# Kernel optimization log

Measured on AMD Instinct MI355X. Metric: run time of the kernel, lower is better.

## Reference

```python
import jax, jax.numpy as jnp
import numpy as np

USER_N = 100000
ITEM_N = 20000
CONCEPT_N = 128
NB_MOD_MAX = 12
M = NB_MOD_MAX + 2  # nb_mod_max_plus_sent
B = 131072


def setup_inputs() -> dict:
    key = jax.random.key(0)
    ks = jax.random.split(key, 6)
    user_ids = jax.random.randint(ks[0], (B,), 0, USER_N)
    item_ids = jax.random.randint(ks[1], (B,), 0, ITEM_N)
    concept_ids = jax.random.randint(ks[2], (B,), 0, CONCEPT_N)
    users_emb_weight = jax.random.normal(ks[3], (USER_N, CONCEPT_N), jnp.float32)
    item_resp_emb_weight = jax.random.normal(ks[4], (ITEM_N * M, CONCEPT_N), jnp.float32)
    # per-item number of modalities in [2, nb_mod_max]
    nb_modalities = jax.random.randint(ks[5], (ITEM_N,), 2, NB_MOD_MAX + 1)
    # mask[item, c] = 0 for c in [1, nb_modalities[item]], +inf elsewhere (matches __init__)
    cols = jnp.arange(M)
    mask = jnp.where((cols[None, :] >= 1) & (cols[None, :] <= nb_modalities[:, None]),
                     0.0, jnp.inf).astype(jnp.float32)
    return dict(user_ids=user_ids, item_ids=item_ids, concept_ids=concept_ids,
                users_emb_weight=users_emb_weight,
                item_resp_emb_weight=item_resp_emb_weight,
                mask=mask, nb_modalities=nb_modalities)


def reference(user_ids, item_ids, concept_ids, users_emb_weight,
              item_resp_emb_weight, mask, nb_modalities):
    m = mask.shape[1]  # nb_mod_max + 2
    # im_idx buffer: item*M + arange(M), then gathered by item_ids
    im_idx = item_ids[:, None] * m + jnp.arange(m)        # [B, M]
    im_emb = item_resp_emb_weight[im_idx]                 # [B, M, C]
    u_emb = users_emb_weight[user_ids]                    # [B, C]
    diff = u_emb[:, None, :] - im_emb                     # [B, M, C]
    p_uim = jnp.sum(diff * diff, axis=2)                  # [B, M]
    idx = jnp.argmin(p_uim + mask[item_ids], axis=1)      # [B]
    nb = nb_modalities[item_ids]                          # [B]
    # mod_to_resp: ((idx - 1) / (nb - 1)) + 1
    return (idx - 1).astype(jnp.float32) / (nb - 1).astype(jnp.float32) + 1.0
```

## Files before the change

kernel.cpp:

```cpp
#include <hip/hip_runtime.h>
#include <math.h>


#define M_TOT 14
#define CDIM 128
#define TAU 0.05f
#define XSTR 68

__global__ void impact_hist(const int* __restrict__ item_ids,
                            int* __restrict__ hist, int B) {
    int i = blockIdx.x * blockDim.x + threadIdx.x;
    int i4 = i * 4;
    if (i4 + 3 < B) {
        int4 v = *(const int4*)(item_ids + i4);
        atomicAdd(&hist[v.x], 1);
        atomicAdd(&hist[v.y], 1);
        atomicAdd(&hist[v.z], 1);
        atomicAdd(&hist[v.w], 1);
    } else {
        for (int k = i4; k < B; ++k) atomicAdd(&hist[item_ids[k]], 1);
    }
}

__global__ __launch_bounds__(256) void impact_scan_part(
    const int* __restrict__ hist, int* __restrict__ cursor,
    int* __restrict__ bsum, int n) {
    __shared__ int sd[256];
    int t = threadIdx.x;
    int k = blockIdx.x * 256 + t;
    int v = (k < n) ? hist[k] : 0;
    sd[t] = v;
    __syncthreads();
#pragma unroll
    for (int off = 1; off < 256; off <<= 1) {
        int x = (t >= off) ? sd[t - off] : 0;
        __syncthreads();
        sd[t] += x;
        __syncthreads();
    }
    if (k < n) cursor[k] = sd[t] - v;
    if (t == 255) bsum[blockIdx.x] = sd[255];
}

__global__ __launch_bounds__(256) void impact_scatter(
    const int* __restrict__ item_ids,
    const int* __restrict__ user_ids,
    const int* __restrict__ nb_mod,
    int* __restrict__ cursor,
    const int* __restrict__ bsum, int nblk,
    int4* __restrict__ s4, int B)
{
    __shared__ int bo[128];
    int t = threadIdx.x;
    int v0 = 0;
    if (t < 128) {
        v0 = (t < nblk) ? bsum[t] : 0;
        bo[t] = v0;
    }
    __syncthreads();
#pragma unroll
    for (int off = 1; off < 128; off <<= 1) {
        int x = (t < 128 && t >= off) ? bo[t - off] : 0;
        __syncthreads();
        if (t < 128) bo[t] += x;
        __syncthreads();
    }
    int ex = (t < 128) ? bo[t] - v0 : 0;
    __syncthreads();
    if (t < 128) bo[t] = ex;
    __syncthreads();

    int i = blockIdx.x * blockDim.x + t;
    int i4 = i * 4;
    if (i4 + 3 < B) {
        int4 it = *(const int4*)(item_ids + i4);
        int4 us = *(const int4*)(user_ids + i4);
        int n0 = nb_mod[it.x], n1 = nb_mod[it.y];
        int n2 = nb_mod[it.z], n3 = nb_mod[it.w];
        int p0 = atomicAdd(&cursor[it.x], 1) + bo[it.x >> 8];
        int p1 = atomicAdd(&cursor[it.y], 1) + bo[it.y >> 8];
        int p2 = atomicAdd(&cursor[it.z], 1) + bo[it.z >> 8];
        int p3 = atomicAdd(&cursor[it.w], 1) + bo[it.w >> 8];
        s4[p0] = make_int4(i4,     us.x, it.x, n0);
        s4[p1] = make_int4(i4 + 1, us.y, it.y, n1);
        s4[p2] = make_int4(i4 + 2, us.z, it.z, n2);
        s4[p3] = make_int4(i4 + 3, us.w, it.w, n3);
    } else {
        for (int k = i4; k < B; ++k) {
            int it = item_ids[k];
            int p = atomicAdd(&cursor[it], 1) + bo[it >> 8];
            s4[p] = make_int4(k, user_ids[k], it, nb_mod[it]);
        }
    }
}

__global__ __launch_bounds__(256) void impact_main(
    const int4* __restrict__ s4,
    const int* __restrict__ user_ids,
    const int* __restrict__ item_ids,
    const int* __restrict__ nb_mod,
    const float* __restrict__ users_emb,
    const float* __restrict__ item_emb,
    float* __restrict__ out,
    int* __restrict__ flag_cnt,
    int* __restrict__ flag_list,
    int B)
{
    __shared__ float xpose[4 * 12 * XSTR];

    int p = blockIdx.x;
    int lb = p;
    if ((gridDim.x & 7) == 0) {
        int cpx = gridDim.x >> 3;
        lb = (p & 7) * cpx + (p >> 3);
    }

    int w = threadIdx.x >> 6;
    int g = (threadIdx.x >> 4) & 3;
    int l = threadIdx.x & 15;
    int qi = lb * 16 + w * 4 + g;

    bool vq = qi < B;
    int4 cur;
    if (s4) {
        cur = vq ? s4[qi] : make_int4(0, 0, 0, 2);
    } else {
        int qq = vq ? qi : 0;
        int ii = item_ids[qq];
        cur = make_int4(qq, user_ids[qq], ii, nb_mod[ii]);
    }
    int q = cur.x, uid = cur.y, iid = cur.z, nb = cur.w;

    const float4* urow = (const float4*)(users_emb + (size_t)uid * CDIM);
    float4 u0 = urow[l];
    float4 u1 = urow[l + 16];
    const float4* vbase =
        (const float4*)(item_emb + ((size_t)iid * M_TOT + 1) * CDIM);
    float* X = xpose + w * 12 * XSTR;

#pragma unroll
    for (int mb = 0; mb < 12; mb += 4) {
        float4 a[4], b[4];
#pragma unroll
        for (int j = 0; j < 4; ++j) {
            int m = mb + j;
            if (m < nb) {
                const float4* vr = vbase + (size_t)m * (CDIM / 4);
                a[j] = vr[l];
                b[j] = vr[l + 16];
            }
        }
#pragma unroll
        for (int j = 0; j < 4; ++j) {
            int m = mb + j;
            if (m < nb) {
                float d0 = u0.x - a[j].x, d1 = u0.y - a[j].y;
                float d2 = u0.z - a[j].z, d3 = u0.w - a[j].w;
                float d4 = u1.x - b[j].x, d5 = u1.y - b[j].y;
                float d6 = u1.z - b[j].z, d7 = u1.w - b[j].w;
                X[m * XSTR + g * 16 + l] =
                    ((d0 * d0 + d1 * d1) + (d2 * d2 + d3 * d3))
                  + ((d4 * d4 + d5 * d5) + (d6 * d6 + d7 * d7));
            }
        }
    }


    int lm = (l < 12) ? l : 0;
    const float4* R4 = (const float4*)(xpose + w * 12 * XSTR + lm * XSTR + g * 16);
    float4 r0 = R4[0], r1 = R4[1], r2 = R4[2], r3 = R4[3];
    float t0 = r0.x + r0.y + r0.z + r0.w;
    float t1 = r1.x + r1.y + r1.z + r1.w;
    float t2 = r2.x + r2.y + r2.z + r2.w;
    float t3 = r3.x + r3.y + r3.z + r3.w;
    float s = (t0 + t1) + (t2 + t3);
    if (l >= nb) s = INFINITY;

    float b1 = s, b2 = INFINITY;
    int i1 = l + 1;
#pragma unroll
    for (int off = 1; off < 16; off <<= 1) {
        float ob1 = __shfl_xor(b1, off);
        float ob2 = __shfl_xor(b2, off);
        int   oi1 = __shfl_xor(i1, off);
        float lo = fminf(b1, ob1);
        float hi = fmaxf(b1, ob1);
        if (ob1 < b1 || (ob1 == b1 && oi1 < i1)) i1 = oi1;
        b1 = lo;
        b2 = fminf(fminf(b2, ob2), hi);
    }

    if (l == 0 && vq) {
        out[q] = (float)(i1 - 1) / (float)(nb - 1) + 1.0f;
        if (b2 - b1 < TAU && flag_cnt) {
            int pos = atomicAdd(flag_cnt, 1);
            flag_list[pos] = q;
        }
    }
}

__global__ __launch_bounds__(256) void impact_refine(
    const int* __restrict__ user_ids,
    const int* __restrict__ item_ids,
    const float* __restrict__ users_emb,
    const float* __restrict__ item_emb,
    const int* __restrict__ nb_mod,
    const int* __restrict__ flag_cnt,
    const int* __restrict__ flag_list,
    float* __restrict__ out)
{
    int cnt = *flag_cnt;
    int ngrp = (gridDim.x * blockDim.x) >> 4;
    int gid = (blockIdx.x * blockDim.x + threadIdx.x) >> 4;
    int l = threadIdx.x & 15;

    for (int i = gid; i < cnt; i += ngrp) {
        int q = flag_list[i];
        int uid = user_ids[q];
        int iid = item_ids[q];
        int nb  = nb_mod[iid];

        const float4* urow = (const float4*)(users_emb + (size_t)uid * CDIM);
        float4 u0 = urow[l];
        float4 u1 = urow[l + 16];

        double best = 1e300;
        int bidx = 1;
        const float4* ibase =
            (const float4*)(item_emb + ((size_t)iid * M_TOT + 1) * CDIM);

        for (int m = 1; m <= nb; ++m) {
            const float4* vr = ibase + (size_t)(m - 1) * (CDIM / 4);
            float4 v0 = vr[l];
            float4 v1 = vr[l + 16];
            float d;
            double sd = 0.0;
            d = u0.x - v0.x; sd += (double)d * d;
            d = u0.y - v0.y; sd += (double)d * d;
            d = u0.z - v0.z; sd += (double)d * d;
            d = u0.w - v0.w; sd += (double)d * d;
            d = u1.x - v1.x; sd += (double)d * d;
            d = u1.y - v1.y; sd += (double)d * d;
            d = u1.z - v1.z; sd += (double)d * d;
            d = u1.w - v1.w; sd += (double)d * d;
            sd += __shfl_xor(sd, 1);
            sd += __shfl_xor(sd, 2);
            sd += __shfl_xor(sd, 4);
            sd += __shfl_xor(sd, 8);
            if (sd < best) { best = sd; bidx = m; }
        }
        if (l == 0)
            out[q] = (float)(bidx - 1) / (float)(nb - 1) + 1.0f;
    }
}

extern "C" void kernel_launch(void* const* d_in, const int* in_sizes, int n_in,
                              void* d_out, int out_size, void* d_ws, size_t ws_size,
                              hipStream_t stream) {
    const int*   user_ids  = (const int*)d_in[0];
    const int*   item_ids  = (const int*)d_in[1];
    const float* users_emb = (const float*)d_in[3];
    const float* item_emb  = (const float*)d_in[4];
    const int*   nb_mod    = (const int*)d_in[6];
    float* out = (float*)d_out;

    int B = in_sizes[0];
    int n_items = in_sizes[6];
    int nblk = (n_items + 255) >> 8;

    size_t need = (size_t)B * 16 + ((size_t)n_items * 2 + 4 + 128 + (size_t)B) * 4;
    int4* s4       = (int4*)d_ws;
    int* hist      = (int*)(s4 + B);
    int* flag_cnt  = hist + n_items;
    int* cursor    = flag_cnt + 4;
    int* bsum      = cursor + n_items;
    int* flag_list = bsum + 128;

    bool sorted = (ws_size >= need) && (nblk <= 128);
    if (sorted) {
        hipMemsetAsync(hist, 0, ((size_t)n_items + 4) * sizeof(int), stream);
        impact_hist<<<(B / 4 + 255) / 256, 256, 0, stream>>>(item_ids, hist, B);
        impact_scan_part<<<nblk, 256, 0, stream>>>(hist, cursor, bsum, n_items);
        impact_scatter<<<(B / 4 + 255) / 256, 256, 0, stream>>>(
            item_ids, user_ids, nb_mod, cursor, bsum, nblk, s4, B);
    }

    int grid = (B + 15) / 16;
    impact_main<<<grid, 256, 0, stream>>>(
        sorted ? s4 : nullptr, user_ids, item_ids, nb_mod,
        users_emb, item_emb, out,
        sorted ? flag_cnt : nullptr, sorted ? flag_list : nullptr, B);

    if (sorted)
        impact_refine<<<64, 256, 0, stream>>>(
            user_ids, item_ids, users_emb, item_emb, nb_mod,
            flag_cnt, flag_list, out);
}
```

Measured before the change: 70.99 us.

## Assign 32 lanes per query instead of 16 in main kernel

Remaps the main distance kernel so each query is handled by 32 lanes, each loading one float4 per modality row, with 8 queries per block and a doubled grid. The shared transpose buffer stride shrinks to fit 32 partials per row. The aim is to spread memory loads over more lanes and raise memory-level parallelism. The cost is fewer registers of work per thread, more blocks, and a heavier reduction per query.

```diff
diff --git a/kernel.cpp b/kernel.cpp
--- a/kernel.cpp
+++ b/kernel.cpp
@@ -5,7 +5,7 @@
 #define M_TOT 14
 #define CDIM 128
 #define TAU 0.05f
-#define XSTR 68
+#define XSTR 36
 
 __global__ void impact_hist(const int* __restrict__ item_ids,
                             int* __restrict__ hist, int B) {
@@ -106,7 +106,7 @@
     int* __restrict__ flag_list,
     int B)
 {
-    __shared__ float xpose[4 * 12 * XSTR];
+    __shared__ float xpose[8 * 12 * XSTR];
 
     int p = blockIdx.x;
     int lb = p;
@@ -115,10 +115,9 @@
         lb = (p & 7) * cpx + (p >> 3);
     }
 
-    int w = threadIdx.x >> 6;
-    int g = (threadIdx.x >> 4) & 3;
-    int l = threadIdx.x & 15;
-    int qi = lb * 16 + w * 4 + g;
+    int grp = threadIdx.x >> 5;
+    int l   = threadIdx.x & 31;
+    int qi = lb * 8 + grp;
 
     bool vq = qi < B;
     int4 cur;
@@ -132,52 +131,49 @@
     int q = cur.x, uid = cur.y, iid = cur.z, nb = cur.w;
 
     const float4* urow = (const float4*)(users_emb + (size_t)uid * CDIM);
-    float4 u0 = urow[l];
-    float4 u1 = urow[l + 16];
+    float4 u = urow[l];
+
     const float4* vbase =
         (const float4*)(item_emb + ((size_t)iid * M_TOT + 1) * CDIM);
-    float* X = xpose + w * 12 * XSTR;
+    float* X = xpose + grp * 12 * XSTR;
 
 #pragma unroll
     for (int mb = 0; mb < 12; mb += 4) {
-        float4 a[4], b[4];
+        float4 a[4];
+#pragma unroll
+        for (int j = 0; j < 4; ++j) {
+            int m = mb + j;
+            if (m < nb) a[j] = vbase[(size_t)m * (CDIM / 4) + l];
+        }
 #pragma unroll
         for (int j = 0; j < 4; ++j) {
             int m = mb + j;
             if (m < nb) {
-                const float4* vr = vbase + (size_t)m * (CDIM / 4);
-                a[j] = vr[l];
-                b[j] = vr[l + 16];
+                float d0 = u.x - a[j].x, d1 = u.y - a[j].y;
+                float d2 = u.z - a[j].z, d3 = u.w - a[j].w;
+                X[m * XSTR + l] = (d0 * d0 + d1 * d1) + (d2 * d2 + d3 * d3);
             }
         }
-#pragma unroll
-        for (int j = 0; j < 4; ++j) {
-            int m = mb + j;
-            if (m < nb) {
-                float d0 = u0.x - a[j].x, d1 = u0.y - a[j].y;
-                float d2 = u0.z - a[j].z, d3 = u0.w - a[j].w;
-                float d4 = u1.x - b[j].x, d5 = u1.y - b[j].y;
-                float d6 = u1.z - b[j].z, d7 = u1.w - b[j].w;
-                X[m * XSTR + g * 16 + l] =
-                    ((d0 * d0 + d1 * d1) + (d2 * d2 + d3 * d3))
-                  + ((d4 * d4 + d5 * d5) + (d6 * d6 + d7 * d7));
-            }
-        }
     }
 
 
     int lm = (l < 12) ? l : 0;
-    const float4* R4 = (const float4*)(xpose + w * 12 * XSTR + lm * XSTR + g * 16);
-    float4 r0 = R4[0], r1 = R4[1], r2 = R4[2], r3 = R4[3];
-    float t0 = r0.x + r0.y + r0.z + r0.w;
-    float t1 = r1.x + r1.y + r1.z + r1.w;
-    float t2 = r2.x + r2.y + r2.z + r2.w;
-    float t3 = r3.x + r3.y + r3.z + r3.w;
+    const float4* R4 = (const float4*)(X + lm * XSTR);
+    float t0 = 0.f, t1 = 0.f, t2 = 0.f, t3 = 0.f;
+#pragma unroll
+    for (int r = 0; r < 2; ++r) {
+        float4 a = R4[r * 4 + 0], b = R4[r * 4 + 1];
+        float4 c = R4[r * 4 + 2], d = R4[r * 4 + 3];
+        t0 += a.x + a.y + a.z + a.w;
+        t1 += b.x + b.y + b.z + b.w;
+        t2 += c.x + c.y + c.z + c.w;
+        t3 += d.x + d.y + d.z + d.w;
+    }
     float s = (t0 + t1) + (t2 + t3);
-    if (l >= nb) s = INFINITY;
+    if (l >= nb || l >= 12) s = INFINITY;
 
     float b1 = s, b2 = INFINITY;
-    int i1 = l + 1;
+    int i1 = (l & 15) + 1;
 #pragma unroll
     for (int off = 1; off < 16; off <<= 1) {
         float ob1 = __shfl_xor(b1, off);
@@ -285,7 +281,7 @@
             item_ids, user_ids, nb_mod, cursor, bsum, nblk, s4, B);
     }
 
-    int grid = (B + 15) / 16;
+    int grid = (B + 7) / 8;
     impact_main<<<grid, 256, 0, stream>>>(
         sorted ? s4 : nullptr, user_ids, item_ids, nb_mod,
         users_emb, item_emb, out,
```

Result: slower. 83.71 us (+17.9%).

## Fuse near-tie refinement into main kernel and skip unused modality chunks per wave

Applied to the files above, without the earlier changes.

Removes the separate refine kernel and the flag list and counter. Near-tie queries are now recomputed in double precision inline, inside the main kernel, reusing the row pointers already loaded. The 12-modality loop is split into three 4-wide chunks, and chunks 2 and 3 run only if some query in the 64-lane wave has that many modalities. This cuts one launch, a memset region and the atomics, but it adds a divergent double-precision loop in the hot kernel and drops __launch_bounds__(256).

```diff
diff --git a/kernel.cpp b/kernel.cpp
--- a/kernel.cpp
+++ b/kernel.cpp
@@ -94,7 +94,7 @@
     }
 }
 
-__global__ __launch_bounds__(256) void impact_main(
+__global__ void impact_main(
     const int4* __restrict__ s4,
     const int* __restrict__ user_ids,
     const int* __restrict__ item_ids,
@@ -102,8 +102,6 @@
     const float* __restrict__ users_emb,
     const float* __restrict__ item_emb,
     float* __restrict__ out,
-    int* __restrict__ flag_cnt,
-    int* __restrict__ flag_list,
     int B)
 {
     __shared__ float xpose[4 * 12 * XSTR];
@@ -138,12 +136,37 @@
         (const float4*)(item_emb + ((size_t)iid * M_TOT + 1) * CDIM);
     float* X = xpose + w * 12 * XSTR;
 
-#pragma unroll
-    for (int mb = 0; mb < 12; mb += 4) {
+    int nbw = max(nb, __shfl_xor(nb, 16));
+    nbw = max(nbw, __shfl_xor(nbw, 32));
+
+    {
         float4 a[4], b[4];
 #pragma unroll
         for (int j = 0; j < 4; ++j) {
-            int m = mb + j;
+            if (j < nb) {
+                const float4* vr = vbase + (size_t)j * (CDIM / 4);
+                a[j] = vr[l];
+                b[j] = vr[l + 16];
+            }
+        }
+#pragma unroll
+        for (int j = 0; j < 4; ++j) {
+            if (j < nb) {
+                float d0 = u0.x - a[j].x, d1 = u0.y - a[j].y;
+                float d2 = u0.z - a[j].z, d3 = u0.w - a[j].w;
+                float d4 = u1.x - b[j].x, d5 = u1.y - b[j].y;
+                float d6 = u1.z - b[j].z, d7 = u1.w - b[j].w;
+                X[j * XSTR + g * 16 + l] =
+                    ((d0 * d0 + d1 * d1) + (d2 * d2 + d3 * d3))
+                  + ((d4 * d4 + d5 * d5) + (d6 * d6 + d7 * d7));
+            }
+        }
+    }
+    if (nbw > 4) {
+        float4 a[4], b[4];
+#pragma unroll
+        for (int j = 0; j < 4; ++j) {
+            int m = 4 + j;
             if (m < nb) {
                 const float4* vr = vbase + (size_t)m * (CDIM / 4);
                 a[j] = vr[l];
@@ -152,7 +175,32 @@
         }
 #pragma unroll
         for (int j = 0; j < 4; ++j) {
-            int m = mb + j;
+            int m = 4 + j;
+            if (m < nb) {
+                float d0 = u0.x - a[j].x, d1 = u0.y - a[j].y;
+                float d2 = u0.z - a[j].z, d3 = u0.w - a[j].w;
+                float d4 = u1.x - b[j].x, d5 = u1.y - b[j].y;
+                float d6 = u1.z - b[j].z, d7 = u1.w - b[j].w;
+                X[m * XSTR + g * 16 + l] =
+                    ((d0 * d0 + d1 * d1) + (d2 * d2 + d3 * d3))
+                  + ((d4 * d4 + d5 * d5) + (d6 * d6 + d7 * d7));
+            }
+        }
+    }
+    if (nbw > 8) {
+        float4 a[4], b[4];
+#pragma unroll
+        for (int j = 0; j < 4; ++j) {
+            int m = 8 + j;
+            if (m < nb) {
+                const float4* vr = vbase + (size_t)m * (CDIM / 4);
+                a[j] = vr[l];
+                b[j] = vr[l + 16];
+            }
+        }
+#pragma unroll
+        for (int j = 0; j < 4; ++j) {
+            int m = 8 + j;
             if (m < nb) {
                 float d0 = u0.x - a[j].x, d1 = u0.y - a[j].y;
                 float d2 = u0.z - a[j].z, d3 = u0.w - a[j].w;
@@ -190,47 +238,12 @@
         b2 = fminf(fminf(b2, ob2), hi);
     }
 
-    if (l == 0 && vq) {
-        out[q] = (float)(i1 - 1) / (float)(nb - 1) + 1.0f;
-        if (b2 - b1 < TAU && flag_cnt) {
-            int pos = atomicAdd(flag_cnt, 1);
-            flag_list[pos] = q;
-        }
-    }
-}
-
-__global__ __launch_bounds__(256) void impact_refine(
-    const int* __restrict__ user_ids,
-    const int* __restrict__ item_ids,
-    const float* __restrict__ users_emb,
-    const float* __restrict__ item_emb,
-    const int* __restrict__ nb_mod,
-    const int* __restrict__ flag_cnt,
-    const int* __restrict__ flag_list,
-    float* __restrict__ out)
-{
-    int cnt = *flag_cnt;
-    int ngrp = (gridDim.x * blockDim.x) >> 4;
-    int gid = (blockIdx.x * blockDim.x + threadIdx.x) >> 4;
-    int l = threadIdx.x & 15;
-
-    for (int i = gid; i < cnt; i += ngrp) {
-        int q = flag_list[i];
-        int uid = user_ids[q];
-        int iid = item_ids[q];
-        int nb  = nb_mod[iid];
-
-        const float4* urow = (const float4*)(users_emb + (size_t)uid * CDIM);
-        float4 u0 = urow[l];
-        float4 u1 = urow[l + 16];
-
+    int idx = i1;
+    if (vq && (b2 - b1 < TAU)) {
         double best = 1e300;
         int bidx = 1;
-        const float4* ibase =
-            (const float4*)(item_emb + ((size_t)iid * M_TOT + 1) * CDIM);
-
         for (int m = 1; m <= nb; ++m) {
-            const float4* vr = ibase + (size_t)(m - 1) * (CDIM / 4);
+            const float4* vr = vbase + (size_t)(m - 1) * (CDIM / 4);
             float4 v0 = vr[l];
             float4 v1 = vr[l + 16];
             float d;
@@ -249,9 +262,11 @@
             sd += __shfl_xor(sd, 8);
             if (sd < best) { best = sd; bidx = m; }
         }
-        if (l == 0)
-            out[q] = (float)(bidx - 1) / (float)(nb - 1) + 1.0f;
-    }
+        idx = bidx;
+    }
+
+    if (l == 0 && vq)
+        out[q] = (float)(idx - 1) / (float)(nb - 1) + 1.0f;
 }
 
 extern "C" void kernel_launch(void* const* d_in, const int* in_sizes, int n_in,
@@ -268,17 +283,15 @@
     int n_items = in_sizes[6];
     int nblk = (n_items + 255) >> 8;
 
-    size_t need = (size_t)B * 16 + ((size_t)n_items * 2 + 4 + 128 + (size_t)B) * 4;
-    int4* s4       = (int4*)d_ws;
-    int* hist      = (int*)(s4 + B);
-    int* flag_cnt  = hist + n_items;
-    int* cursor    = flag_cnt + 4;
-    int* bsum      = cursor + n_items;
-    int* flag_list = bsum + 128;
+    size_t need = (size_t)B * 16 + ((size_t)n_items * 2 + 128) * 4;
+    int4* s4   = (int4*)d_ws;
+    int* hist  = (int*)(s4 + B);
+    int* cursor = hist + n_items;
+    int* bsum  = cursor + n_items;
 
     bool sorted = (ws_size >= need) && (nblk <= 128);
     if (sorted) {
-        hipMemsetAsync(hist, 0, ((size_t)n_items + 4) * sizeof(int), stream);
+        hipMemsetAsync(hist, 0, (size_t)n_items * sizeof(int), stream);
         impact_hist<<<(B / 4 + 255) / 256, 256, 0, stream>>>(item_ids, hist, B);
         impact_scan_part<<<nblk, 256, 0, stream>>>(hist, cursor, bsum, n_items);
         impact_scatter<<<(B / 4 + 255) / 256, 256, 0, stream>>>(
@@ -288,11 +301,5 @@
     int grid = (B + 15) / 16;
     impact_main<<<grid, 256, 0, stream>>>(
         sorted ? s4 : nullptr, user_ids, item_ids, nb_mod,
-        users_emb, item_emb, out,
-        sorted ? flag_cnt : nullptr, sorted ? flag_list : nullptr, B);
-
-    if (sorted)
-        impact_refine<<<64, 256, 0, stream>>>(
-            user_ids, item_ids, users_emb, item_emb, nb_mod,
-            flag_cnt, flag_list, out);
-}
+        users_emb, item_emb, out, B);
+}
```

New measurement: 58.66 us. -17.4%, faster.
